# Kernel tuning notes

Hardware: AMD Instinct MI355X
Metric: run time of the kernel (lower is better)

## Reference

```python
import jax, jax.numpy as jnp
import numpy as np

N_NODES = 100000
N_EDGES = 1600000
D_IN = 64
D_OUT = 64


def setup_inputs() -> dict:
    key = jax.random.key(0)
    k1, k2, k3, k4, k5, k6 = jax.random.split(key, 6)
    x = jax.random.normal(k1, (N_NODES, D_IN), dtype=jnp.float32)
    weight = jax.random.normal(k2, (D_IN, D_OUT), dtype=jnp.float32) * (1.0 / np.sqrt(D_OUT))
    bias = jax.random.normal(k3, (D_OUT,), dtype=jnp.float32) * (1.0 / np.sqrt(D_OUT))
    adj_vals = jax.random.uniform(k4, (N_EDGES,), dtype=jnp.float32)
    src = jax.random.randint(k5, (N_EDGES,), 0, N_NODES, dtype=jnp.int32)
    dst = jax.random.randint(k6, (N_EDGES,), 0, N_NODES, dtype=jnp.int32)
    return {"x": x, "weight": weight, "bias": bias, "adj_vals": adj_vals, "src": src, "dst": dst}


def reference(x, weight, bias, adj_vals, src, dst):
    # support = X @ W  -> [N, D_OUT]
    support = jnp.dot(x, weight)
    # sparse adjacency matmul: out[dst] += adj_vals * support[src]
    msgs = adj_vals[:, None] * support[src]  # [E, D_OUT]
    out = jax.ops.segment_sum(msgs, dst, num_segments=N_NODES)
    return out + bias
```

## Files before the change

### kernel.cpp

```cpp
#include <hip/hip_runtime.h>

#define N_NODES 100000
#define N_EDGES 1600000
#define D 64

#define BN 64
#define NBUCK ((N_NODES + BN - 1) / BN)
#define CHW 256
#define CH ((N_EDGES + CHW - 1) / CHW)
#define CITER 13
#define SMAX 2048
#define OVF 512
#define PAD 16

static __device__ __forceinline__ unsigned short f2bf(float f) {
    unsigned u = __float_as_uint(f);
    u += 0x7FFFu + ((u >> 16) & 1u);
    return (unsigned short)(u >> 16);
}
static __device__ __forceinline__ float bf2f(unsigned short h) {
    return __uint_as_float((unsigned)h << 16);
}

__global__ __launch_bounds__(256) void gcn_gemm(const float* __restrict__ x,
                                                const float* __restrict__ w,
                                                unsigned short* __restrict__ support) {
    __shared__ float4 wsh[64 * 16];
    int tid = threadIdx.x;
    const float4* w4 = (const float4*)w;
    for (int i = tid; i < 64 * 16; i += 256) wsh[i] = w4[i];
    __syncthreads();

    int idx = blockIdx.x * 256 + tid;
    int rowpair = idx >> 4;
    int c4 = idx & 15;
    long r0 = (long)rowpair * 2;
    const float4* xr0 = (const float4*)(x + r0 * D);
    const float4* xr1 = (const float4*)(x + (r0 + 1) * D);

    float4 a0 = make_float4(0.f, 0.f, 0.f, 0.f);
    float4 a1 = make_float4(0.f, 0.f, 0.f, 0.f);
    #pragma unroll 4
    for (int k4 = 0; k4 < 16; ++k4) {
        float4 xv0 = xr0[k4];
        float4 xv1 = xr1[k4];
        float4 w0 = wsh[(4 * k4 + 0) * 16 + c4];
        float4 w1 = wsh[(4 * k4 + 1) * 16 + c4];
        float4 w2 = wsh[(4 * k4 + 2) * 16 + c4];
        float4 w3 = wsh[(4 * k4 + 3) * 16 + c4];
        a0 += w0 * xv0.x + w1 * xv0.y + w2 * xv0.z + w3 * xv0.w;
        a1 += w0 * xv1.x + w1 * xv1.y + w2 * xv1.z + w3 * xv1.w;
    }
    ushort4* s4 = (ushort4*)support;
    s4[r0 * 16 + c4] = make_ushort4(f2bf(a0.x), f2bf(a0.y), f2bf(a0.z), f2bf(a0.w));
    s4[(r0 + 1) * 16 + c4] = make_ushort4(f2bf(a1.x), f2bf(a1.y), f2bf(a1.z), f2bf(a1.w));
}

__global__ __launch_bounds__(512) void gcn_bcount(const int* __restrict__ dst,
                                                  int* __restrict__ btot) {
    __shared__ int h[NBUCK];
    int tid = threadIdx.x;
    for (int i = tid; i < NBUCK; i += 512) h[i] = 0;
    __syncthreads();
    int e0 = blockIdx.x * CH, e1 = min(e0 + CH, N_EDGES);
    for (int e = e0 + tid; e < e1; e += 512) {
        int d = __builtin_nontemporal_load(&dst[e]);
        atomicAdd(&h[d >> 6], 1);
    }
    __syncthreads();
    for (int i = tid; i < NBUCK; i += 512)
        if (h[i]) atomicAdd(&btot[i * PAD], h[i]);
}

__global__ __launch_bounds__(1024) void gcn_bscan(const int* __restrict__ btot,
                                                  int* __restrict__ sbase,
                                                  int* __restrict__ gcur) {
    __shared__ int sh[1024];
    int tid = threadIdx.x;
    int i0 = 2 * tid, i1 = 2 * tid + 1;
    int t0 = (i0 < NBUCK) ? btot[i0 * PAD] : 0;
    int t1 = (i1 < NBUCK) ? btot[i1 * PAD] : 0;
    int local = t0 + t1;
    sh[tid] = local;
    __syncthreads();
    for (int off = 1; off < 1024; off <<= 1) {
        int t = 0;
        if (tid >= off) t = sh[tid - off];
        __syncthreads();
        if (tid >= off) sh[tid] += t;
        __syncthreads();
    }
    int excl = sh[tid] - local;
    if (i0 < NBUCK) { sbase[i0] = excl;      gcur[i0 * PAD] = excl; }
    if (i1 < NBUCK) { sbase[i1] = excl + t0; gcur[i1 * PAD] = excl + t0; }
    if (tid == 1023) sbase[NBUCK] = sh[1023];
}

__global__ __launch_bounds__(512) void gcn_coarse(const int* __restrict__ src,
                                                  const int* __restrict__ dst,
                                                  const float* __restrict__ adj,
                                                  int* __restrict__ gcur,
                                                  int2* __restrict__ coarse) {
    __shared__ int h[NBUCK];
    __shared__ int cur[NBUCK];
    int tid = threadIdx.x, w = blockIdx.x;
    for (int i = tid; i < NBUCK; i += 512) h[i] = 0;
    __syncthreads();

    int e0 = w * CH, e1 = min(e0 + CH, N_EDGES);
    int dreg[CITER], sreg[CITER];
    float areg[CITER];
    #pragma unroll
    for (int it = 0; it < CITER; ++it) {
        int e = e0 + tid + it * 512;
        dreg[it] = -1;
        if (e < e1) {
            dreg[it] = __builtin_nontemporal_load(&dst[e]);
            sreg[it] = __builtin_nontemporal_load(&src[e]);
            areg[it] = __builtin_nontemporal_load(&adj[e]);
            atomicAdd(&h[dreg[it] >> 6], 1);
        }
    }
    __syncthreads();

    for (int c = tid; c < NBUCK; c += 512) {
        int hc = h[c];
        if (hc) cur[c] = atomicAdd(&gcur[c * PAD], hc);
    }
    __syncthreads();

    #pragma unroll
    for (int it = 0; it < CITER; ++it) {
        if (dreg[it] >= 0) {
            int c = dreg[it] >> 6;
            int pos = atomicAdd(&cur[c], 1);
            coarse[pos] = make_int2(sreg[it] | ((dreg[it] & 63) << 17),
                                    __float_as_int(areg[it]));
        }
    }
}

__global__ __launch_bounds__(256) void gcn_bgather(const unsigned short* __restrict__ support,
                                                   const int2* __restrict__ coarse,
                                                   const int* __restrict__ sbase,
                                                   const float* __restrict__ bias,
                                                   float* __restrict__ out) {
    __shared__ int2 sE[SMAX];
    __shared__ int2 ovfE[OVF];
    __shared__ int cntS[BN], loffS[BN], curS[BN];
    __shared__ int ovfN;

    int tid = threadIdx.x, wv = tid >> 6, lane = tid & 63;
    int b = blockIdx.x;
    int e0 = sbase[b];
    int e1 = sbase[b + 1];

    if (tid < BN) cntS[tid] = 0;
    if (tid == 0) ovfN = 0;
    __syncthreads();

    for (int e = e0 + tid; e < e1; e += 256)
        atomicAdd(&cntS[(coarse[e].x >> 17) & 63], 1);
    __syncthreads();

    if (tid < BN) loffS[tid] = cntS[tid];
    __syncthreads();
    for (int off = 1; off < BN; off <<= 1) {
        int t = 0;
        if (tid < BN && tid >= off) t = loffS[tid - off];
        __syncthreads();
        if (tid < BN && tid >= off) loffS[tid] += t;
        __syncthreads();
    }
    if (tid < BN) {
        int excl = loffS[tid] - cntS[tid];
        loffS[tid] = excl;
        curS[tid] = excl;
    }
    __syncthreads();

    for (int e = e0 + tid; e < e1; e += 256) {
        int2 ed = coarse[e];
        int nl = (ed.x >> 17) & 63;
        int pos = atomicAdd(&curS[nl], 1);
        if (pos < SMAX) sE[pos] = ed;
        else {
            int op = atomicAdd(&ovfN, 1);
            if (op < OVF) ovfE[op] = ed;
        }
    }
    __syncthreads();

    int eg = lane >> 4;
    int L  = lane & 15;
    const uint2* sup2 = (const uint2*)support;
    const float4* bias4 = (const float4*)bias;
    float4* out4 = (float4*)out;
    float4 bv = bias4[L];

    for (int nl = wv * 16; nl < wv * 16 + 16; ++nl) {
        int start = loffS[nl], cnt = cntS[nl];
        int endc = min(start + cnt, SMAX);
        int avail = endc > start ? endc - start : 0;
        float4 acc = make_float4(0.f, 0.f, 0.f, 0.f);
        for (int j = 0; j < avail; j += 16) {
            #pragma unroll
            for (int q = 0; q < 4; ++q) {
                int ei = j + q * 4 + eg;
                int2 ed = sE[start + min(ei, avail - 1)];
                float wgt = (ei < avail) ? __int_as_float(ed.y) : 0.f;
                uint2 p = sup2[(long)(ed.x & 0x1FFFF) * 16 + L];
                acc.x += wgt * __uint_as_float(p.x << 16);
                acc.y += wgt * __uint_as_float(p.x & 0xFFFF0000u);
                acc.z += wgt * __uint_as_float(p.y << 16);
                acc.w += wgt * __uint_as_float(p.y & 0xFFFF0000u);
            }
        }
        acc.x += __shfl_xor(acc.x, 16, 64); acc.y += __shfl_xor(acc.y, 16, 64);
        acc.z += __shfl_xor(acc.z, 16, 64); acc.w += __shfl_xor(acc.w, 16, 64);
        acc.x += __shfl_xor(acc.x, 32, 64); acc.y += __shfl_xor(acc.y, 32, 64);
        acc.z += __shfl_xor(acc.z, 32, 64); acc.w += __shfl_xor(acc.w, 32, 64);
        int n = b * BN + nl;
        if (lane < 16 && n < N_NODES) {
            float4 r = make_float4(acc.x + bv.x, acc.y + bv.y,
                                   acc.z + bv.z, acc.w + bv.w);
            out4[(long)n * 16 + L] = r;
        }
    }

    __syncthreads();
    int no = min(ovfN, OVF);
    for (int i = wv; i < no; i += 4) {
        int2 ed = ovfE[i];
        int s = ed.x & 0x1FFFF, dl = (ed.x >> 17) & 63;
        int n = b * BN + dl;
        if (n < N_NODES) {
            float v = __int_as_float(ed.y) * bf2f(support[(long)s * D + lane]);
            atomicAdd(&out[(long)n * D + lane], v);
        }
    }
}

extern "C" void kernel_launch(void* const* d_in, const int* in_sizes, int n_in,
                              void* d_out, int out_size, void* d_ws, size_t ws_size,
                              hipStream_t stream) {
    const float* x      = (const float*)d_in[0];
    const float* weight = (const float*)d_in[1];
    const float* bias   = (const float*)d_in[2];
    const float* adj    = (const float*)d_in[3];
    const int*   src    = (const int*)d_in[4];
    const int*   dst    = (const int*)d_in[5];
    float* out = (float*)d_out;

    unsigned short* support = (unsigned short*)d_ws;
    int2* coarse = (int2*)(support + (long)N_NODES * D);
    int*  btot   = (int*)(coarse + N_EDGES);
    int*  gcur   = btot + NBUCK * PAD;
    int*  sbase  = gcur + NBUCK * PAD;

    hipLaunchKernelGGL(gcn_gemm, dim3(N_NODES * 16 / 2 / 256), dim3(256), 0, stream,
                       x, weight, support);
    hipMemsetAsync(btot, 0, NBUCK * PAD * sizeof(int), stream);
    hipLaunchKernelGGL(gcn_bcount, dim3(CHW), dim3(512), 0, stream, dst, btot);
    hipLaunchKernelGGL(gcn_bscan, dim3(1), dim3(1024), 0, stream, btot, sbase, gcur);
    hipLaunchKernelGGL(gcn_coarse, dim3(CHW), dim3(512), 0, stream,
                       src, dst, adj, gcur, coarse);
    hipLaunchKernelGGL(gcn_bgather, dim3(NBUCK), dim3(256), 0, stream,
                       support, coarse, sbase, bias, out);
}
```

Before: 212.2 us.

## Fuse bucket count, scan and binning into one cooperative kernel

Replaces the separate bucket-count, single-block scan and coarse-binning kernels with one cooperative kernel that uses grid-wide syncs. Edge indices are loaded only once instead of twice, and two launches disappear. The kernel also accumulates per-node degree counts with global atomics, which lets the gather kernel skip its per-bucket counting pass over the coarse edges. In exchange it adds 1.6M global atomics on ncnt, two grid barriers, and a dependency on cooperative launch residency.

```diff
diff --git a/kernel.cpp b/kernel.cpp
--- a/kernel.cpp
+++ b/kernel.cpp
@@ -1,4 +1,7 @@
 #include <hip/hip_runtime.h>
+#include <hip/hip_cooperative_groups.h>
+
+namespace cg = cooperative_groups;
 
 #define N_NODES 100000
 #define N_EDGES 1600000
@@ -56,53 +59,17 @@
     s4[(r0 + 1) * 16 + c4] = make_ushort4(f2bf(a1.x), f2bf(a1.y), f2bf(a1.z), f2bf(a1.w));
 }
 
-__global__ __launch_bounds__(512) void gcn_bcount(const int* __restrict__ dst,
-                                                  int* __restrict__ btot) {
-    __shared__ int h[NBUCK];
-    int tid = threadIdx.x;
-    for (int i = tid; i < NBUCK; i += 512) h[i] = 0;
-    __syncthreads();
-    int e0 = blockIdx.x * CH, e1 = min(e0 + CH, N_EDGES);
-    for (int e = e0 + tid; e < e1; e += 512) {
-        int d = __builtin_nontemporal_load(&dst[e]);
-        atomicAdd(&h[d >> 6], 1);
-    }
-    __syncthreads();
-    for (int i = tid; i < NBUCK; i += 512)
-        if (h[i]) atomicAdd(&btot[i * PAD], h[i]);
-}
-
-__global__ __launch_bounds__(1024) void gcn_bscan(const int* __restrict__ btot,
-                                                  int* __restrict__ sbase,
-                                                  int* __restrict__ gcur) {
-    __shared__ int sh[1024];
-    int tid = threadIdx.x;
-    int i0 = 2 * tid, i1 = 2 * tid + 1;
-    int t0 = (i0 < NBUCK) ? btot[i0 * PAD] : 0;
-    int t1 = (i1 < NBUCK) ? btot[i1 * PAD] : 0;
-    int local = t0 + t1;
-    sh[tid] = local;
-    __syncthreads();
-    for (int off = 1; off < 1024; off <<= 1) {
-        int t = 0;
-        if (tid >= off) t = sh[tid - off];
-        __syncthreads();
-        if (tid >= off) sh[tid] += t;
-        __syncthreads();
-    }
-    int excl = sh[tid] - local;
-    if (i0 < NBUCK) { sbase[i0] = excl;      gcur[i0 * PAD] = excl; }
-    if (i1 < NBUCK) { sbase[i1] = excl + t0; gcur[i1 * PAD] = excl + t0; }
-    if (tid == 1023) sbase[NBUCK] = sh[1023];
-}
-
-__global__ __launch_bounds__(512) void gcn_coarse(const int* __restrict__ src,
+__global__ __launch_bounds__(512, 2) void gcn_bin(const int* __restrict__ src,
                                                   const int* __restrict__ dst,
                                                   const float* __restrict__ adj,
+                                                  int* __restrict__ ncnt,
+                                                  int* __restrict__ btot,
+                                                  int* __restrict__ sbase,
                                                   int* __restrict__ gcur,
                                                   int2* __restrict__ coarse) {
     __shared__ int h[NBUCK];
     __shared__ int cur[NBUCK];
+    __shared__ int psc[512];
     int tid = threadIdx.x, w = blockIdx.x;
     for (int i = tid; i < NBUCK; i += 512) h[i] = 0;
     __syncthreads();
@@ -118,10 +85,41 @@
             dreg[it] = __builtin_nontemporal_load(&dst[e]);
             sreg[it] = __builtin_nontemporal_load(&src[e]);
             areg[it] = __builtin_nontemporal_load(&adj[e]);
+            atomicAdd(&ncnt[dreg[it]], 1);
             atomicAdd(&h[dreg[it] >> 6], 1);
         }
     }
     __syncthreads();
+    for (int c = tid; c < NBUCK; c += 512)
+        if (h[c]) atomicAdd(&btot[c], h[c]);
+
+    cg::this_grid().sync();
+
+    if (w == 0) {
+        int b0 = tid * 4;
+        int v0 = (b0     < NBUCK) ? atomicAdd(&btot[b0    ], 0) : 0;
+        int v1 = (b0 + 1 < NBUCK) ? atomicAdd(&btot[b0 + 1], 0) : 0;
+        int v2 = (b0 + 2 < NBUCK) ? atomicAdd(&btot[b0 + 2], 0) : 0;
+        int v3 = (b0 + 3 < NBUCK) ? atomicAdd(&btot[b0 + 3], 0) : 0;
+        int s = v0 + v1 + v2 + v3;
+        psc[tid] = s;
+        __syncthreads();
+        for (int off = 1; off < 512; off <<= 1) {
+            int t = 0;
+            if (tid >= off) t = psc[tid - off];
+            __syncthreads();
+            if (tid >= off) psc[tid] += t;
+            __syncthreads();
+        }
+        int run = psc[tid] - s;
+        if (b0     < NBUCK) { sbase[b0    ] = run; atomicExch(&gcur[(b0    ) * PAD], run); } run += v0;
+        if (b0 + 1 < NBUCK) { sbase[b0 + 1] = run; atomicExch(&gcur[(b0 + 1) * PAD], run); } run += v1;
+        if (b0 + 2 < NBUCK) { sbase[b0 + 2] = run; atomicExch(&gcur[(b0 + 2) * PAD], run); } run += v2;
+        if (b0 + 3 < NBUCK) { sbase[b0 + 3] = run; atomicExch(&gcur[(b0 + 3) * PAD], run); } run += v3;
+        if (tid == 511) sbase[NBUCK] = run;
+    }
+
+    cg::this_grid().sync();
 
     for (int c = tid; c < NBUCK; c += 512) {
         int hc = h[c];
@@ -143,6 +141,7 @@
 __global__ __launch_bounds__(256) void gcn_bgather(const unsigned short* __restrict__ support,
                                                    const int2* __restrict__ coarse,
                                                    const int* __restrict__ sbase,
+                                                   const int* __restrict__ ncnt,
                                                    const float* __restrict__ bias,
                                                    float* __restrict__ out) {
     __shared__ int2 sE[SMAX];
@@ -155,12 +154,11 @@
     int e0 = sbase[b];
     int e1 = sbase[b + 1];
 
-    if (tid < BN) cntS[tid] = 0;
+    if (tid < BN) {
+        int n = b * BN + tid;
+        cntS[tid] = (n < N_NODES) ? ncnt[n] : 0;
+    }
     if (tid == 0) ovfN = 0;
-    __syncthreads();
-
-    for (int e = e0 + tid; e < e1; e += 256)
-        atomicAdd(&cntS[(coarse[e].x >> 17) & 63], 1);
     __syncthreads();
 
     if (tid < BN) loffS[tid] = cntS[tid];
@@ -254,17 +252,17 @@
 
     unsigned short* support = (unsigned short*)d_ws;
     int2* coarse = (int2*)(support + (long)N_NODES * D);
-    int*  btot   = (int*)(coarse + N_EDGES);
-    int*  gcur   = btot + NBUCK * PAD;
-    int*  sbase  = gcur + NBUCK * PAD;
+    int*  ncnt   = (int*)(coarse + N_EDGES);
+    int*  btot   = ncnt + N_NODES;
+    int*  sbase  = btot + NBUCK;
+    int*  gcur   = sbase + (NBUCK + 1);
 
     hipLaunchKernelGGL(gcn_gemm, dim3(N_NODES * 16 / 2 / 256), dim3(256), 0, stream,
                        x, weight, support);
-    hipMemsetAsync(btot, 0, NBUCK * PAD * sizeof(int), stream);
-    hipLaunchKernelGGL(gcn_bcount, dim3(CHW), dim3(512), 0, stream, dst, btot);
-    hipLaunchKernelGGL(gcn_bscan, dim3(1), dim3(1024), 0, stream, btot, sbase, gcur);
-    hipLaunchKernelGGL(gcn_coarse, dim3(CHW), dim3(512), 0, stream,
-                       src, dst, adj, gcur, coarse);
+    hipMemsetAsync(ncnt, 0, (N_NODES + NBUCK) * sizeof(int), stream);
+    void* args[] = {(void*)&src, (void*)&dst, (void*)&adj, (void*)&ncnt,
+                    (void*)&btot, (void*)&sbase, (void*)&gcur, (void*)&coarse};
+    hipLaunchCooperativeKernel((void*)gcn_bin, dim3(CHW), dim3(512), args, 0, stream);
     hipLaunchKernelGGL(gcn_bgather, dim3(NBUCK), dim3(256), 0, stream,
-                       support, coarse, sbase, bias, out);
-}
+                       support, coarse, sbase, ncnt, bias, out);
+}
```

After: 326.5 us. +53.8%, slower.
